# Kernel optimization log

Measured on AMD Instinct MI355X. Metric: run time of the kernel, lower is better.

The kernel has to match this reference:

```python
import jax, jax.numpy as jnp
import numpy as np

B, H, L, D = 2, 16, 1024, 64
LMAX = 2048  # max_sequence_length: patterns built & normalized at LMAX, then sliced to L
PI = float(np.pi)


def _scale_pattern(freq):
    # pattern[h, t, d] = exp(i(t+ph)) + exp(i(2t+ph)) + exp(i(0.5t+ph)), ph = 2*pi*h/H
    # identical across d, so keep [H, L, 1] and broadcast over D
    phase = 2.0 * PI * jnp.arange(H, dtype=jnp.float32) / H          # [H]
    t = jnp.linspace(0.0, 2.0 * PI * freq, LMAX)                     # [LMAX]
    a1 = t[None, :] + phase[:, None]
    a2 = 2.0 * t[None, :] + phase[:, None]
    a3 = 0.5 * t[None, :] + phase[:, None]
    pr = jnp.cos(a1) + jnp.cos(a2) + jnp.cos(a3)                     # [H, LMAX]
    pi_ = jnp.sin(a1) + jnp.sin(a2) + jnp.sin(a3)
    norm = jnp.sqrt(jnp.sum(pr * pr + pi_ * pi_, axis=1, keepdims=True))  # over full LMAX
    pr, pi_ = pr / norm, pi_ / norm
    return pr[:, :L, None], pi_[:, :L, None]                          # [H, L, 1]


def _expert_total_pattern():
    # 8 experts x 3 aspects; pattern[t, d] = exp(i(f*t + 2*pi*d/D)), normalized per
    # column over LMAX (|exp|=1 -> norm sqrt(LMAX)). Elementwise complex multiply is
    # linear, so the expert stage equals x * sum(all patterns)/(sqrt(3)*sqrt(8)).
    freqs = np.array([[0.3 + 0.1 * i, 0.2 + 0.1 * i, 0.1 + 0.1 * i]
                      for i in range(8)], dtype=np.float32).reshape(-1)   # [24]
    t = jnp.linspace(0.0, 2.0 * PI, LMAX)                                 # [LMAX]
    phase_d = 2.0 * PI * jnp.arange(D, dtype=jnp.float32) / D             # [D]
    ang = jnp.asarray(freqs)[:, None, None] * t[None, :, None] + phase_d[None, None, :]  # [24, LMAX, D]
    col_norm = 1.0 / np.sqrt(float(LMAX))
    denom = np.sqrt(3.0) * np.sqrt(8.0)
    pr = jnp.sum(jnp.cos(ang), axis=0) * (col_norm / denom)               # [LMAX, D]
    pi_ = jnp.sum(jnp.sin(ang), axis=0) * (col_norm / denom)
    return pr[:L], pi_[:L]                                                # [L, D]


def _process_scale(Qr, Qi, Kr, Ki, Vr, Vi, pr, pi_):
    # complex elementwise pattern multiply
    Qpr = Qr * pr - Qi * pi_
    Qpi = Qr * pi_ + Qi * pr
    Kpr = Kr * pr - Ki * pi_
    Kpi = Kr * pi_ + Ki * pr
    # complex scores = Qp @ Kp^T (no conjugation, matching the torch code)
    sr = jnp.einsum('bhld,bhmd->bhlm', Qpr, Kpr) - jnp.einsum('bhld,bhmd->bhlm', Qpi, Kpi)
    si = jnp.einsum('bhld,bhmd->bhlm', Qpr, Kpi) + jnp.einsum('bhld,bhmd->bhlm', Qpi, Kpr)
    mag = jnp.sqrt(sr * sr + si * si) / np.sqrt(float(D))
    w = jax.nn.softmax(mag, axis=-1)
    return (jnp.einsum('bhlm,bhmd->bhld', w, Vr),
            jnp.einsum('bhlm,bhmd->bhld', w, Vi))


def reference(Q_real, Q_imag, K_real, K_imag, V_real, V_imag):
    scale_freqs = [1.0, 0.5, 0.25, 0.1]  # char, word, phrase, sentence
    acc_r = jnp.zeros_like(Q_real)
    acc_i = jnp.zeros_like(Q_real)
    for f in scale_freqs:
        pr, pi_ = _scale_pattern(f)
        o_r, o_i = _process_scale(Q_real, Q_imag, K_real, K_imag, V_real, V_imag, pr, pi_)
        acc_r = acc_r + o_r
        acc_i = acc_i + o_i
    inv = 1.0 / np.sqrt(float(len(scale_freqs)))
    acc_r = acc_r * inv
    acc_i = acc_i * inv
    # expert mixing (linear in x -> single fused complex elementwise multiply)
    epr, epi = _expert_total_pattern()  # [L, D], broadcast over B,H
    out_r = acc_r * epr - acc_i * epi
    out_i = acc_r * epi + acc_i * epr
    return jnp.stack([out_r, out_i], axis=0)  # [2, B, H, L, D] (real, imag)


def setup_inputs() -> dict:
    key = jax.random.key(0)
    ks = jax.random.split(key, 6)
    shape = (B, H, L, D)
    names = ['Q_real', 'Q_imag', 'K_real', 'K_imag', 'V_real', 'V_imag']
    return {n: jax.random.normal(k, shape, dtype=jnp.float32) for n, k in zip(names, ks)}
```

## Files before the change

kernel.cpp:

```cpp
#include <hip/hip_runtime.h>
#include <math.h>

typedef short bf16x8 __attribute__((ext_vector_type(8)));
typedef float f32x4 __attribute__((ext_vector_type(4)));

#define BDIM 256
#define ADIM 1024
constexpr int B_ = 2, H_ = 16, L_ = 1024, D_ = 64, LMAX_ = 2048;
constexpr int BH_ = B_ * H_;
constexpr float PI_F = 3.14159265358979323846f;

constexpr int WS_SVP = 0;
constexpr int WS_KBR = 65536;
constexpr int WS_KBI = WS_KBR + 1048576;
constexpr int WS_VTR = WS_KBI + 1048576;
constexpr int WS_VTI = WS_VTR + 1048576;

__device__ __forceinline__ unsigned short f2b(float x) {
    union { float f; unsigned u; } v; v.f = x;
    return (unsigned short)((v.u + 0x8000u) >> 16);
}
__device__ __forceinline__ float b2f(unsigned short x) {
    union { unsigned u; float f; } v; v.u = ((unsigned)x) << 16;
    return v.f;
}
__device__ __forceinline__ unsigned pk2(float a, float b) {
    union { float f; unsigned u; } va, vb; va.f = a; vb.f = b;
    return ((va.u + 0x8000u) >> 16) | ((vb.u + 0x8000u) & 0xFFFF0000u);
}
__device__ __forceinline__ uint4 pack4(const float4& a, const float4& b) {
    return make_uint4(pk2(a.x, a.y), pk2(a.z, a.w), pk2(b.x, b.y), pk2(b.z, b.w));
}
__device__ __forceinline__ unsigned cvtpk(float lo, float hi) {
    unsigned r;
    asm("v_cvt_pk_bf16_f32 %0, %1, %2" : "=v"(r) : "v"(lo), "v"(hi));
    return r;
}
__device__ __forceinline__ float vsqrt(float x) {
    float r;
    asm("v_sqrt_f32 %0, %1" : "=v"(r) : "v"(x));
    return r;
}

#define MFMA(a, b, c) __builtin_amdgcn_mfma_f32_16x16x32_bf16((a), (b), (c), 0, 0, 0)

__device__ __forceinline__ float a_val(int s, int l, float4 invn) {
    const float fr = (s == 0) ? 1.0f : (s == 1) ? 0.5f : (s == 2) ? 0.25f : 0.1f;
    const float iv = (s == 0) ? invn.x : (s == 1) ? invn.y : (s == 2) ? invn.z : invn.w;
    float t = (2.0f * PI_F * fr / (float)(LMAX_ - 1)) * (float)l;
    float m2 = 3.0f + 2.0f * cosf(t) + 2.0f * cosf(0.5f * t) + 2.0f * cosf(1.5f * t);
    return sqrtf(fmaxf(m2, 0.0f)) * iv;
}

__global__ __launch_bounds__(BDIM)
void prep_kernel(const float* __restrict__ Kr, const float* __restrict__ Ki,
                 const float* __restrict__ Vr, const float* __restrict__ Vi,
                 float* __restrict__ ws) {
    const int tid = threadIdx.x;
    const int blk = blockIdx.x;
    unsigned short* KbR = (unsigned short*)(ws + WS_KBR);
    unsigned short* KbI = (unsigned short*)(ws + WS_KBI);
    unsigned short* VtR = (unsigned short*)(ws + WS_VTR);
    unsigned short* VtI = (unsigned short*)(ws + WS_VTI);

    if (blk < 256) {
        const int comp = blk >> 7;
        const float* src = comp ? Ki : Kr;
        unsigned short* dst = comp ? KbI : KbR;
        size_t b0 = (size_t)(blk & 127) * 16384;
#pragma unroll
        for (int i = 0; i < 4; ++i) {
            size_t e = b0 + (size_t)(i * 256 + tid) * 16;
            float4 x0 = *(const float4*)(src + e);
            float4 x1 = *(const float4*)(src + e + 4);
            float4 x2 = *(const float4*)(src + e + 8);
            float4 x3 = *(const float4*)(src + e + 12);
            *(uint4*)(dst + e) = pack4(x0, x1);
            *(uint4*)(dst + e + 8) = pack4(x2, x3);
        }
    } else {
        __shared__ unsigned short sT[64 * 70];
        __shared__ float sRed[4 * 64];
        const int vb = blk - 256;
        const int comp = vb & 1, mt = (vb >> 1) & 15, bh = vb >> 5;
        const int m0 = mt * 64;
        const float* src = (comp ? Vi : Vr) + (size_t)bh * 65536 + (size_t)m0 * 64;
        unsigned short* dstA = (comp ? VtI : VtR) + (size_t)bh * 65536;
#pragma unroll
        for (int i = 0; i < 4; ++i) {
            int e = i * 256 + tid;
            int m = e >> 4, d4 = (e & 15) * 4;
            float4 x = *(const float4*)(src + (size_t)m * 64 + d4);
            *(uint2*)&sT[m * 70 + d4] = make_uint2(pk2(x.x, x.y), pk2(x.z, x.w));
        }
        {
            int d = tid & 63, grp = tid >> 6;
            float s = 0.0f;
#pragma unroll
            for (int k = 0; k < 16; ++k) s += src[(size_t)(grp * 16 + k) * 64 + d];
            sRed[grp * 64 + d] = s;
        }
        __syncthreads();
        {
            int d = tid >> 2, ms = (tid & 3) * 16;
            unsigned short v[16];
#pragma unroll
            for (int k = 0; k < 16; ++k) v[k] = sT[(ms + k) * 70 + d];
            unsigned short* dst = dstA + (size_t)d * 1024 + m0 + ms;
            *(uint4*)dst = make_uint4((unsigned)v[0] | ((unsigned)v[1] << 16),
                                      (unsigned)v[2] | ((unsigned)v[3] << 16),
                                      (unsigned)v[4] | ((unsigned)v[5] << 16),
                                      (unsigned)v[6] | ((unsigned)v[7] << 16));
            *(uint4*)(dst + 8) = make_uint4((unsigned)v[8] | ((unsigned)v[9] << 16),
                                            (unsigned)v[10] | ((unsigned)v[11] << 16),
                                            (unsigned)v[12] | ((unsigned)v[13] << 16),
                                            (unsigned)v[14] | ((unsigned)v[15] << 16));
        }
        if (tid < 64)
            ws[WS_SVP + comp * 32768 + bh * 1024 + tid * 16 + mt] =
                sRed[tid] + sRed[64 + tid] + sRed[128 + tid] + sRed[192 + tid];
    }
}

__device__ __forceinline__ void stage64s(const unsigned short* g0, int stride,
                                         unsigned short* lds, int w, int lane) {
#pragma unroll
    for (int i = 0; i < 2; ++i) {
        int c = w * 2 + i;
        int lrow = c * 8 + (lane >> 3);
        int lg = (lane & 7) ^ (lrow & 7);
        const unsigned short* src = g0 + (size_t)lrow * stride + lg * 8;
        __builtin_amdgcn_global_load_lds(
            (const __attribute__((address_space(1))) void*)src,
            (__attribute__((address_space(3))) void*)(lds + c * 512), 16, 0, 0);
    }
}
__device__ __forceinline__ bf16x8 ldfrag(const unsigned short* b, int row, int g) {
    return *(const bf16x8*)&b[row * 64 + ((g ^ (row & 7)) << 3)];
}

constexpr int OFF_DEN = 0;
constexpr int OFF_K0  = 2048;
constexpr int OFF_K1  = OFF_K0 + 16384;
constexpr int OFF_V0  = OFF_K1 + 16384;
constexpr int OFF_V1  = OFF_V0 + 16384;
constexpr int OFF_E   = OFF_V1 + 16384;
constexpr int OFF_MG  = OFF_E + 16384;
constexpr int OFF_AMB = OFF_MG + 16384;
constexpr int SMEM_BYTES = OFF_AMB + 8256;

__global__ __launch_bounds__(ADIM, 1)
void attn_kernel_w(const float* __restrict__ Qr, const float* __restrict__ Qi,
                   const float* __restrict__ ws, float* __restrict__ out, float4 invn) {
    extern __shared__ char smem[];
    float* sDen = (float*)(smem + OFF_DEN);
    unsigned short* sK0 = (unsigned short*)(smem + OFF_K0);
    unsigned short* sK1 = (unsigned short*)(smem + OFF_K1);
    unsigned short* sV0 = (unsigned short*)(smem + OFF_V0);
    unsigned short* sV1 = (unsigned short*)(smem + OFF_V1);
    unsigned short* sE  = (unsigned short*)(smem + OFF_E);
    unsigned short* sMg = (unsigned short*)(smem + OFF_MG);
    unsigned short* sAmb = (unsigned short*)(smem + OFF_AMB);

    const int tid = threadIdx.x;
    const int lane = tid & 63;
    const int w = tid >> 6;
    const int half = w >> 3;
    const int w8 = w & 7;
    const int lo16 = lane & 15;
    const int quad = lane >> 4;
    const int gh = quad + half * 4;
    const int blk = blockIdx.x;
    const int bh = (blk & 7) * 4 + (blk >> 6);
    const int qt = (blk >> 3) & 7;
    const int l0 = qt * 128;
    const size_t base = (size_t)bh * (L_ * D_);

    const unsigned short* gKr = (const unsigned short*)(ws + WS_KBR) + (size_t)bh * 65536;
    const unsigned short* gKi = (const unsigned short*)(ws + WS_KBI) + (size_t)bh * 65536;
    const unsigned short* gVr = (const unsigned short*)(ws + WS_VTR) + (size_t)bh * 65536;
    const unsigned short* gVi = (const unsigned short*)(ws + WS_VTI) + (size_t)bh * 65536;

    if (w < 4) {
        stage64s(gKr, 64, sK0, w, lane);
        stage64s(gKi, 64, sK1, w, lane);
    } else if (w >= 8 && w < 12) {
        stage64s(gVr, 1024, sV0, w - 8, lane);
        stage64s(gVi, 1024, sV1, w - 8, lane);
    }

    for (int e = tid; e < 4096; e += ADIM) {
        int s = e >> 10, l = e & 1023;
        sAmb[s * 1032 + l] = f2b(a_val(s, l, invn) * 0.125f);
    }

    bf16x8 fQr0, fQr1, fQi0, fQi1, fnQi0, fnQi1;
    {
        const int ql = l0 + w8 * 16 + lo16;
        const float* qr = Qr + base + (size_t)ql * 64;
        const float* qi = Qi + base + (size_t)ql * 64;
        float4 a0 = *(const float4*)(qr + quad * 8);
        float4 a1 = *(const float4*)(qr + quad * 8 + 4);
        float4 b0 = *(const float4*)(qr + 32 + quad * 8);
        float4 b1 = *(const float4*)(qr + 32 + quad * 8 + 4);
        *(uint4*)&fQr0 = pack4(a0, a1);
        *(uint4*)&fQr1 = pack4(b0, b1);
        a0 = *(const float4*)(qi + quad * 8);
        a1 = *(const float4*)(qi + quad * 8 + 4);
        b0 = *(const float4*)(qi + 32 + quad * 8);
        b1 = *(const float4*)(qi + 32 + quad * 8 + 4);
        *(uint4*)&fQi0 = pack4(a0, a1);
        *(uint4*)&fQi1 = pack4(b0, b1);
        uint4 t0 = *(uint4*)&fQi0, t1 = *(uint4*)&fQi1;
        t0.x ^= 0x80008000u; t0.y ^= 0x80008000u; t0.z ^= 0x80008000u; t0.w ^= 0x80008000u;
        t1.x ^= 0x80008000u; t1.y ^= 0x80008000u; t1.z ^= 0x80008000u; t1.w ^= 0x80008000u;
        *(uint4*)&fnQi0 = t0; *(uint4*)&fnQi1 = t1;
    }

    __syncthreads();

    bf16x8 uf1a = (bf16x8){0, 0, 0, 0, 0, 0, 0, 0};
    uf1a[0] = (short)f2b(b2f(sAmb[quad * 1032 + (l0 + w8 * 16 + lo16)]) *
                         (1.0f / 128.0f));

    f32x4 accM1 = (f32x4){0.f, 0.f, 0.f, 0.f};
    f32x4 aOutR[4], aOutI[4];
#pragma unroll
    for (int dt = 0; dt < 4; ++dt) {
        aOutR[dt] = (f32x4){0.f, 0.f, 0.f, 0.f};
        aOutI[dt] = (f32x4){0.f, 0.f, 0.f, 0.f};
    }

    const int lrow_w = w8 * 16 + lo16;

#pragma unroll 1
    for (int mt = 0; mt < 16; ++mt) {
        const int m0 = mt * 64;
        const int cur = mt & 1;
        if (mt < 15) {
            if (w < 4) {
                stage64s(gKr + (size_t)(m0 + 64) * 64, 64, sK0 + (cur ^ 1) * 4096, w, lane);
                stage64s(gKi + (size_t)(m0 + 64) * 64, 64, sK1 + (cur ^ 1) * 4096, w, lane);
            } else if (w >= 8 && w < 12) {
                stage64s(gVr + m0 + 64, 1024, sV0 + (cur ^ 1) * 4096, w - 8, lane);
                stage64s(gVi + m0 + 64, 1024, sV1 + (cur ^ 1) * 4096, w - 8, lane);
            }
        }
        const unsigned short* cK0 = sK0 + cur * 4096;
        const unsigned short* cK1 = sK1 + cur * 4096;
        const unsigned short* cV0 = sV0 + cur * 4096;
        const unsigned short* cV1 = sV1 + cur * 4096;

#pragma unroll
        for (int ct = 0; ct < 2; ++ct) {
            const int ct_eff = half * 2 + ct;
            const int mrow = ct_eff * 16 + lo16;
            bf16x8 kr0 = ldfrag(cK0, mrow, quad), kr1 = ldfrag(cK0, mrow, quad + 4);
            bf16x8 ki0 = ldfrag(cK1, mrow, quad), ki1 = ldfrag(cK1, mrow, quad + 4);
            f32x4 aR = (f32x4){0.f, 0.f, 0.f, 0.f};
            f32x4 aI = (f32x4){0.f, 0.f, 0.f, 0.f};
            __builtin_amdgcn_s_setprio(1);
            aR = MFMA(kr0, fQr0, aR);  aR = MFMA(kr1, fQr1, aR);
            aR = MFMA(ki0, fnQi0, aR); aR = MFMA(ki1, fnQi1, aR);
            aI = MFMA(ki0, fQr0, aI);  aI = MFMA(ki1, fQr1, aI);
            aI = MFMA(kr0, fQi0, aI);  aI = MFMA(kr1, fQi1, aI);
            __builtin_amdgcn_s_setprio(0);
            float mg0 = vsqrt(fmaf(aR[0], aR[0], aI[0] * aI[0]));
            float mg1 = vsqrt(fmaf(aR[1], aR[1], aI[1] * aI[1]));
            float mg2 = vsqrt(fmaf(aR[2], aR[2], aI[2] * aI[2]));
            float mg3 = vsqrt(fmaf(aR[3], aR[3], aI[3] * aI[3]));
            bf16x8 bf1 = (bf16x8){0, 0, 0, 0, 0, 0, 0, 0};
            bf1[0] = (short)sAmb[quad * 1032 + m0 + ct_eff * 16 + lo16];
            f32x4 z = (f32x4){0.f, 0.f, 0.f, 0.f};
            f32x4 a1 = MFMA(bf1, uf1a, z);
            float p0 = mg0 * a1[0], p1 = mg1 * a1[1];
            float p2 = mg2 * a1[2], p3 = mg3 * a1[3];
            int gph = (ct_eff * 2 + (quad >> 1)) ^ (lrow_w & 7);
            *(uint2*)&sE[lrow_w * 64 + gph * 8 + (quad & 1) * 4] =
                make_uint2(cvtpk(p0, p1), cvtpk(p2, p3));
            *(uint2*)&sMg[lrow_w * 64 + gph * 8 + (quad & 1) * 4] =
                make_uint2(cvtpk(mg0, mg1), cvtpk(mg2, mg3));
        }
        {
            bf16x8 mf = ldfrag(sMg, lrow_w, gh);
            bf16x8 b0 = (bf16x8){0, 0, 0, 0, 0, 0, 0, 0};
            if (lo16 < 4)
                b0 = *(const bf16x8*)&sAmb[lo16 * 1032 + m0 + half * 32 + quad * 8];
            accM1 = MFMA(mf, b0, accM1);
        }
        {
            bf16x8 pa = ldfrag(sE, lrow_w, gh);
            __builtin_amdgcn_s_setprio(1);
#pragma unroll
            for (int dt = 0; dt < 4; ++dt) {
                int dr = dt * 16 + lo16;
                bf16x8 vr = ldfrag(cV0, dr, gh);
                bf16x8 vi = ldfrag(cV1, dr, gh);
                aOutR[dt] = MFMA(pa, vr, aOutR[dt]);
                aOutI[dt] = MFMA(pa, vi, aOutI[dt]);
            }
            __builtin_amdgcn_s_setprio(0);
        }
        asm volatile("s_waitcnt vmcnt(0)" ::: "memory");
        __builtin_amdgcn_s_barrier();
    }

    char* scr = smem + OFF_K0;
    if (half == 1) {
#pragma unroll
        for (int dt = 0; dt < 4; ++dt) {
            *(f32x4*)(scr + w8 * 9216 + dt * 1024 + lane * 16) = aOutR[dt];
            *(f32x4*)(scr + w8 * 9216 + 4096 + dt * 1024 + lane * 16) = aOutI[dt];
        }
        *(f32x4*)(scr + w8 * 9216 + 8192 + lane * 16) = accM1;
    }
    __syncthreads();
    if (half == 1) return;

#pragma unroll
    for (int dt = 0; dt < 4; ++dt) {
        aOutR[dt] += *(const f32x4*)(scr + w8 * 9216 + dt * 1024 + lane * 16);
        aOutI[dt] += *(const f32x4*)(scr + w8 * 9216 + 4096 + dt * 1024 + lane * 16);
    }
    accM1 += *(const f32x4*)(scr + w8 * 9216 + 8192 + lane * 16);

    if (lo16 < 4) {
#pragma unroll
        for (int reg = 0; reg < 4; ++reg) {
            int r = w8 * 16 + quad * 4 + reg;
            float alv = b2f(sAmb[lo16 * 1032 + (l0 + r)]) * 8.0f;
            sDen[lo16 * 128 + r] = 1.0f / (1024.0f + alv * accM1[reg]);
        }
    }
    float cden[4];
#pragma unroll
    for (int reg = 0; reg < 4; ++reg) {
        int r = w8 * 16 + quad * 4 + reg;
        cden[reg] = sDen[r] + sDen[128 + r] + sDen[256 + r] + sDen[384 + r];
    }

    const float cE = rsqrtf(2048.0f) * rsqrtf(24.0f);
    float eRr[4], eRi[4];
#pragma unroll
    for (int reg = 0; reg < 4; ++reg) {
        int lrow = l0 + w8 * 16 + quad * 4 + reg;
        float tl = (2.0f * PI_F / (float)(LMAX_ - 1)) * (float)lrow;
        float s1, c1;
        __sincosf(0.1f * tl, &s1, &c1);
        const float W[10] = {1.f, 2.f, 3.f, 3.f, 3.f, 3.f, 3.f, 3.f, 2.f, 1.f};
        float cr = c1, ci = s1;
        float er = W[0] * cr, ei = W[0] * ci;
#pragma unroll
        for (int k = 1; k < 10; ++k) {
            float nr = cr * c1 - ci * s1;
            float ni = cr * s1 + ci * c1;
            cr = nr; ci = ni;
            er = fmaf(W[k], cr, er);
            ei = fmaf(W[k], ci, ei);
        }
        eRr[reg] = er * cE;
        eRi[reg] = ei * cE;
    }

    const size_t ooff = (size_t)BH_ * L_ * D_;
#pragma unroll
    for (int dt = 0; dt < 4; ++dt) {
        int d = dt * 16 + lo16;
        const float* svp = ws + WS_SVP + bh * 1024 + (size_t)d * 16;
        float4 r0 = *(const float4*)(svp);
        float4 r1 = *(const float4*)(svp + 4);
        float4 r2 = *(const float4*)(svp + 8);
        float4 r3 = *(const float4*)(svp + 12);
        float svr = (r0.x + r0.y + r0.z + r0.w) + (r1.x + r1.y + r1.z + r1.w) +
                    (r2.x + r2.y + r2.z + r2.w) + (r3.x + r3.y + r3.z + r3.w);
        const float* svq = svp + 32768;
        r0 = *(const float4*)(svq);
        r1 = *(const float4*)(svq + 4);
        r2 = *(const float4*)(svq + 8);
        r3 = *(const float4*)(svq + 12);
        float svi = (r0.x + r0.y + r0.z + r0.w) + (r1.x + r1.y + r1.z + r1.w) +
                    (r2.x + r2.y + r2.z + r2.w) + (r3.x + r3.y + r3.z + r3.w);
        float sp, cp;
        __sincosf((2.0f * PI_F / 64.0f) * (float)d, &sp, &cp);
#pragma unroll
        for (int reg = 0; reg < 4; ++reg) {
            int lrow = l0 + w8 * 16 + quad * 4 + reg;
            float numR = fmaf(cden[reg], svr, aOutR[dt][reg]) * 0.5f;
            float numI = fmaf(cden[reg], svi, aOutI[dt][reg]) * 0.5f;
            float epr = cp * eRr[reg] - sp * eRi[reg];
            float epi = sp * eRr[reg] + cp * eRi[reg];
            size_t o = base + (size_t)lrow * 64 + d;
            out[o] = numR * epr - numI * epi;
            out[o + ooff] = numR * epi + numI * epr;
        }
    }
}

__global__ __launch_bounds__(BDIM, 2)
void attn_kernel(const float* __restrict__ Qr, const float* __restrict__ Qi,
                 const float* __restrict__ ws, float* __restrict__ out, float4 invn) {
    __shared__ unsigned short sK0[2][4096], sK1[2][4096];
    __shared__ unsigned short sV0[4096], sV1[4096];
    __shared__ unsigned short sE[4096];
    __shared__ unsigned short sMg[4096];
    __shared__ unsigned short sAmb[4 * 1032];
    __shared__ float sDen[4 * 64];

    const int tid = threadIdx.x;
    const int lane = tid & 63;
    const int w = tid >> 6;
    const int lo16 = lane & 15;
    const int quad = lane >> 4;
    const int blk = blockIdx.x;
    const int bh = (blk & 7) * 4 + (blk >> 7);
    const int qt = (blk >> 3) & 15;
    const int l0 = qt * 64;
    const size_t base = (size_t)bh * (L_ * D_);

    const unsigned short* gKr = (const unsigned short*)(ws + WS_KBR) + (size_t)bh * 65536;
    const unsigned short* gKi = (const unsigned short*)(ws + WS_KBI) + (size_t)bh * 65536;
    const unsigned short* gVr = (const unsigned short*)(ws + WS_VTR) + (size_t)bh * 65536;
    const unsigned short* gVi = (const unsigned short*)(ws + WS_VTI) + (size_t)bh * 65536;

    stage64s(gKr, 64, sK0[0], w, lane);
    stage64s(gKi, 64, sK1[0], w, lane);

    for (int e = tid; e < 4096; e += BDIM) {
        int s = e >> 10, l = e & 1023;
        sAmb[s * 1032 + l] = f2b(a_val(s, l, invn) * 0.125f);
    }

    bf16x8 fQr0, fQr1, fQi0, fQi1, fnQi0, fnQi1;
    {
        const int ql = l0 + w * 16 + lo16;
        const float* qr = Qr + base + (size_t)ql * 64;
        const float* qi = Qi + base + (size_t)ql * 64;
        float4 a0 = *(const float4*)(qr + quad * 8);
        float4 a1 = *(const float4*)(qr + quad * 8 + 4);
        float4 b0 = *(const float4*)(qr + 32 + quad * 8);
        float4 b1 = *(const float4*)(qr + 32 + quad * 8 + 4);
        *(uint4*)&fQr0 = pack4(a0, a1);
        *(uint4*)&fQr1 = pack4(b0, b1);
        a0 = *(const float4*)(qi + quad * 8);
        a1 = *(const float4*)(qi + quad * 8 + 4);
        b0 = *(const float4*)(qi + 32 + quad * 8);
        b1 = *(const float4*)(qi + 32 + quad * 8 + 4);
        *(uint4*)&fQi0 = pack4(a0, a1);
        *(uint4*)&fQi1 = pack4(b0, b1);
        uint4 t0 = *(uint4*)&fQi0, t1 = *(uint4*)&fQi1;
        t0.x ^= 0x80008000u; t0.y ^= 0x80008000u; t0.z ^= 0x80008000u; t0.w ^= 0x80008000u;
        t1.x ^= 0x80008000u; t1.y ^= 0x80008000u; t1.z ^= 0x80008000u; t1.w ^= 0x80008000u;
        *(uint4*)&fnQi0 = t0; *(uint4*)&fnQi1 = t1;
    }

    __syncthreads();

    bf16x8 uf1a = (bf16x8){0, 0, 0, 0, 0, 0, 0, 0};
    uf1a[0] = (short)f2b(b2f(sAmb[quad * 1032 + (l0 + w * 16 + lo16)]) *
                         (1.0f / 128.0f));

    f32x4 accM1 = (f32x4){0.f, 0.f, 0.f, 0.f};
    f32x4 aOutR[4], aOutI[4];
#pragma unroll
    for (int dt = 0; dt < 4; ++dt) {
        aOutR[dt] = (f32x4){0.f, 0.f, 0.f, 0.f};
        aOutI[dt] = (f32x4){0.f, 0.f, 0.f, 0.f};
    }

#pragma unroll 1
    for (int mt = 0; mt < 16; ++mt) {
        const int m0 = mt * 64;
        const int cur = mt & 1;
        stage64s(gVr + m0, 1024, sV0, w, lane);
        stage64s(gVi + m0, 1024, sV1, w, lane);
        if (mt < 15) {
            stage64s(gKr + (size_t)(m0 + 64) * 64, 64, sK0[cur ^ 1], w, lane);
            stage64s(gKi + (size_t)(m0 + 64) * 64, 64, sK1[cur ^ 1], w, lane);
        }
        const unsigned short* cK0 = sK0[cur];
        const unsigned short* cK1 = sK1[cur];

#pragma unroll
        for (int ct = 0; ct < 4; ++ct) {
            const int mrow = ct * 16 + lo16;
            bf16x8 kr0 = ldfrag(cK0, mrow, quad), kr1 = ldfrag(cK0, mrow, quad + 4);
            bf16x8 ki0 = ldfrag(cK1, mrow, quad), ki1 = ldfrag(cK1, mrow, quad + 4);
            f32x4 aR = (f32x4){0.f, 0.f, 0.f, 0.f};
            f32x4 aI = (f32x4){0.f, 0.f, 0.f, 0.f};
            __builtin_amdgcn_s_setprio(1);
            aR = MFMA(kr0, fQr0, aR);  aR = MFMA(kr1, fQr1, aR);
            aR = MFMA(ki0, fnQi0, aR); aR = MFMA(ki1, fnQi1, aR);
            aI = MFMA(ki0, fQr0, aI);  aI = MFMA(ki1, fQr1, aI);
            aI = MFMA(kr0, fQi0, aI);  aI = MFMA(kr1, fQi1, aI);
            __builtin_amdgcn_s_setprio(0);
            float mg0 = vsqrt(fmaf(aR[0], aR[0], aI[0] * aI[0]));
            float mg1 = vsqrt(fmaf(aR[1], aR[1], aI[1] * aI[1]));
            float mg2 = vsqrt(fmaf(aR[2], aR[2], aI[2] * aI[2]));
            float mg3 = vsqrt(fmaf(aR[3], aR[3], aI[3] * aI[3]));
            bf16x8 bf1 = (bf16x8){0, 0, 0, 0, 0, 0, 0, 0};
            bf1[0] = (short)sAmb[quad * 1032 + m0 + ct * 16 + lo16];
            f32x4 z = (f32x4){0.f, 0.f, 0.f, 0.f};
            f32x4 a1 = MFMA(bf1, uf1a, z);
            float p0 = mg0 * a1[0], p1 = mg1 * a1[1];
            float p2 = mg2 * a1[2], p3 = mg3 * a1[3];
            int l = w * 16 + lo16;
            int gph = (ct * 2 + (quad >> 1)) ^ (l & 7);
            *(uint2*)&sE[l * 64 + gph * 8 + (quad & 1) * 4] =
                make_uint2(cvtpk(p0, p1), cvtpk(p2, p3));
            *(uint2*)&sMg[l * 64 + gph * 8 + (quad & 1) * 4] =
                make_uint2(cvtpk(mg0, mg1), cvtpk(mg2, mg3));
        }
        {
            bf16x8 mf0 = ldfrag(sMg, w * 16 + lo16, quad);
            bf16x8 mf1 = ldfrag(sMg, w * 16 + lo16, quad + 4);
            bf16x8 b0 = (bf16x8){0, 0, 0, 0, 0, 0, 0, 0};
            bf16x8 b1 = (bf16x8){0, 0, 0, 0, 0, 0, 0, 0};
            if (lo16 < 4) {
                b0 = *(const bf16x8*)&sAmb[lo16 * 1032 + m0 + quad * 8];
                b1 = *(const bf16x8*)&sAmb[lo16 * 1032 + m0 + 32 + quad * 8];
            }
            accM1 = MFMA(mf0, b0, accM1);
            accM1 = MFMA(mf1, b1, accM1);
        }
        if (mt < 15) {
            asm volatile("s_waitcnt vmcnt(4)" ::: "memory");
        } else {
            asm volatile("s_waitcnt vmcnt(0)" ::: "memory");
        }
        __builtin_amdgcn_s_barrier();
        {
            bf16x8 pa0 = ldfrag(sE, w * 16 + lo16, quad);
            bf16x8 pa1 = ldfrag(sE, w * 16 + lo16, quad + 4);
            __builtin_amdgcn_s_setprio(1);
#pragma unroll
            for (int dt = 0; dt < 4; ++dt) {
                int dr = dt * 16 + lo16;
                bf16x8 vr0 = ldfrag(sV0, dr, quad), vr1 = ldfrag(sV0, dr, quad + 4);
                bf16x8 vi0 = ldfrag(sV1, dr, quad), vi1 = ldfrag(sV1, dr, quad + 4);
                aOutR[dt] = MFMA(pa0, vr0, aOutR[dt]);
                aOutR[dt] = MFMA(pa1, vr1, aOutR[dt]);
                aOutI[dt] = MFMA(pa0, vi0, aOutI[dt]);
                aOutI[dt] = MFMA(pa1, vi1, aOutI[dt]);
            }
            __builtin_amdgcn_s_setprio(0);
        }
        asm volatile("s_waitcnt vmcnt(0)" ::: "memory");
        __builtin_amdgcn_s_barrier();
    }

    if (lo16 < 4) {
#pragma unroll
        for (int reg = 0; reg < 4; ++reg) {
            int r = w * 16 + quad * 4 + reg;
            float alv = b2f(sAmb[lo16 * 1032 + (l0 + r)]) * 8.0f;
            sDen[lo16 * 64 + r] = 1.0f / (1024.0f + alv * accM1[reg]);
        }
    }
    float cden[4];
#pragma unroll
    for (int reg = 0; reg < 4; ++reg) {
        int r = w * 16 + quad * 4 + reg;
        cden[reg] = sDen[r] + sDen[64 + r] + sDen[128 + r] + sDen[192 + r];
    }

    const float cE = rsqrtf(2048.0f) * rsqrtf(24.0f);
    float eRr[4], eRi[4];
#pragma unroll
    for (int reg = 0; reg < 4; ++reg) {
        int lrow = l0 + w * 16 + quad * 4 + reg;
        float tl = (2.0f * PI_F / (float)(LMAX_ - 1)) * (float)lrow;
        float s1, c1;
        __sincosf(0.1f * tl, &s1, &c1);
        const float W[10] = {1.f, 2.f, 3.f, 3.f, 3.f, 3.f, 3.f, 3.f, 2.f, 1.f};
        float cr = c1, ci = s1;
        float er = W[0] * cr, ei = W[0] * ci;
#pragma unroll
        for (int k = 1; k < 10; ++k) {
            float nr = cr * c1 - ci * s1;
            float ni = cr * s1 + ci * c1;
            cr = nr; ci = ni;
            er = fmaf(W[k], cr, er);
            ei = fmaf(W[k], ci, ei);
        }
        eRr[reg] = er * cE;
        eRi[reg] = ei * cE;
    }

    const size_t ooff = (size_t)BH_ * L_ * D_;
#pragma unroll
    for (int dt = 0; dt < 4; ++dt) {
        int d = dt * 16 + lo16;
        const float* svp = ws + WS_SVP + bh * 1024 + (size_t)d * 16;
        float4 r0 = *(const float4*)(svp);
        float4 r1 = *(const float4*)(svp + 4);
        float4 r2 = *(const float4*)(svp + 8);
        float4 r3 = *(const float4*)(svp + 12);
        float svr = (r0.x + r0.y + r0.z + r0.w) + (r1.x + r1.y + r1.z + r1.w) +
                    (r2.x + r2.y + r2.z + r2.w) + (r3.x + r3.y + r3.z + r3.w);
        const float* svq = svp + 32768;
        r0 = *(const float4*)(svq);
        r1 = *(const float4*)(svq + 4);
        r2 = *(const float4*)(svq + 8);
        r3 = *(const float4*)(svq + 12);
        float svi = (r0.x + r0.y + r0.z + r0.w) + (r1.x + r1.y + r1.z + r1.w) +
                    (r2.x + r2.y + r2.z + r2.w) + (r3.x + r3.y + r3.z + r3.w);
        float sp, cp;
        __sincosf((2.0f * PI_F / 64.0f) * (float)d, &sp, &cp);
#pragma unroll
        for (int reg = 0; reg < 4; ++reg) {
            int lrow = l0 + w * 16 + quad * 4 + reg;
            float numR = fmaf(cden[reg], svr, aOutR[dt][reg]) * 0.5f;
            float numI = fmaf(cden[reg], svi, aOutI[dt][reg]) * 0.5f;
            float epr = cp * eRr[reg] - sp * eRi[reg];
            float epi = sp * eRr[reg] + cp * eRi[reg];
            size_t o = base + (size_t)lrow * 64 + d;
            out[o] = numR * epr - numI * epi;
            out[o + ooff] = numR * epi + numI * epr;
        }
    }
}

extern "C" void kernel_launch(void* const* d_in, const int* in_sizes, int n_in,
                              void* d_out, int out_size, void* d_ws, size_t ws_size,
                              hipStream_t stream) {
    const float* Qr = (const float*)d_in[0];
    const float* Qi = (const float*)d_in[1];
    const float* Kr = (const float*)d_in[2];
    const float* Ki = (const float*)d_in[3];
    const float* Vr = (const float*)d_in[4];
    const float* Vi = (const float*)d_in[5];
    float* ws = (float*)d_ws;
    float* out = (float*)d_out;

    const double fr[4] = {1.0, 0.5, 0.25, 0.1};
    float inv[4];
    for (int s = 0; s < 4; ++s) {
        double a = 2.0 * 3.14159265358979323846 * fr[s] / (double)(LMAX_ - 1);
        double S = 3.0 * LMAX_;
        const double mul[3] = {1.0, 0.5, 1.5};
        for (int k = 0; k < 3; ++k) {
            double x = a * mul[k];
            S += 2.0 * (cos(x * 1023.5) * sin(x * 1024.0) / sin(x * 0.5));
        }
        inv[s] = (float)(1.0 / sqrt(S));
    }
    float4 invn = make_float4(inv[0], inv[1], inv[2], inv[3]);

    prep_kernel<<<1280, BDIM, 0, stream>>>(Kr, Ki, Vr, Vi, ws);

    static int wideOK = -1;
    if (wideOK < 0) {
        hipError_t e = hipFuncSetAttribute(
            reinterpret_cast<const void*>(attn_kernel_w),
            hipFuncAttributeMaxDynamicSharedMemorySize, SMEM_BYTES);
        wideOK = (e == hipSuccess) ? 1 : 0;
    }
    if (wideOK)
        attn_kernel_w<<<256, ADIM, SMEM_BYTES, stream>>>(Qr, Qi, ws, out, invn);
    else
        attn_kernel<<<512, BDIM, 0, stream>>>(Qr, Qi, ws, out, invn);
}
```

Baseline: 134.6 us.

## Halve workgroup to 8 waves, each wave handling two 16-row query subtiles

The wide attention kernel drops from 16 waves to 8 waves per workgroup, and each wave now processes two 16-row query slices. That lets one loaded K fragment and one loaded V fragment feed twice as many MFMAs. Launch bounds now ask for 2 workgroups per CU, so two blocks may be resident at once. The trade-off is roughly doubled accumulator register pressure per wave (two sets of output and score accumulators), which risks spills or lower effective occupancy.

```diff
diff --git a/kernel.cpp b/kernel.cpp
--- a/kernel.cpp
+++ b/kernel.cpp
@@ -5,7 +5,7 @@
 typedef float f32x4 __attribute__((ext_vector_type(4)));
 
 #define BDIM 256
-#define ADIM 1024
+#define ADIM 512
 constexpr int B_ = 2, H_ = 16, L_ = 1024, D_ = 64, LMAX_ = 2048;
 constexpr int BH_ = B_ * H_;
 constexpr float PI_F = 3.14159265358979323846f;
@@ -149,7 +149,7 @@
 constexpr int OFF_AMB = OFF_MG + 16384;
 constexpr int SMEM_BYTES = OFF_AMB + 8256;
 
-__global__ __launch_bounds__(ADIM, 1)
+__global__ __launch_bounds__(ADIM, 2)
 void attn_kernel_w(const float* __restrict__ Qr, const float* __restrict__ Qi,
                    const float* __restrict__ ws, float* __restrict__ out, float4 invn) {
     extern __shared__ char smem[];
@@ -165,8 +165,8 @@
     const int tid = threadIdx.x;
     const int lane = tid & 63;
     const int w = tid >> 6;
-    const int half = w >> 3;
-    const int w8 = w & 7;
+    const int half = w >> 2;
+    const int w4 = w & 3;
     const int lo16 = lane & 15;
     const int quad = lane >> 4;
     const int gh = quad + half * 4;
@@ -184,9 +184,9 @@
     if (w < 4) {
         stage64s(gKr, 64, sK0, w, lane);
         stage64s(gKi, 64, sK1, w, lane);
-    } else if (w >= 8 && w < 12) {
-        stage64s(gVr, 1024, sV0, w - 8, lane);
-        stage64s(gVi, 1024, sV1, w - 8, lane);
+    } else {
+        stage64s(gVr, 1024, sV0, w - 4, lane);
+        stage64s(gVi, 1024, sV1, w - 4, lane);
     }
 
     for (int e = tid; e < 4096; e += ADIM) {
@@ -194,44 +194,51 @@
         sAmb[s * 1032 + l] = f2b(a_val(s, l, invn) * 0.125f);
     }
 
-    bf16x8 fQr0, fQr1, fQi0, fQi1, fnQi0, fnQi1;
-    {
-        const int ql = l0 + w8 * 16 + lo16;
+    bf16x8 fQr0[2], fQr1[2], fQi0[2], fQi1[2], fnQi0[2], fnQi1[2];
+#pragma unroll
+    for (int qs = 0; qs < 2; ++qs) {
+        const int ql = l0 + w4 * 32 + qs * 16 + lo16;
         const float* qr = Qr + base + (size_t)ql * 64;
         const float* qi = Qi + base + (size_t)ql * 64;
         float4 a0 = *(const float4*)(qr + quad * 8);
         float4 a1 = *(const float4*)(qr + quad * 8 + 4);
         float4 b0 = *(const float4*)(qr + 32 + quad * 8);
         float4 b1 = *(const float4*)(qr + 32 + quad * 8 + 4);
-        *(uint4*)&fQr0 = pack4(a0, a1);
-        *(uint4*)&fQr1 = pack4(b0, b1);
+        *(uint4*)&fQr0[qs] = pack4(a0, a1);
+        *(uint4*)&fQr1[qs] = pack4(b0, b1);
         a0 = *(const float4*)(qi + quad * 8);
         a1 = *(const float4*)(qi + quad * 8 + 4);
         b0 = *(const float4*)(qi + 32 + quad * 8);
         b1 = *(const float4*)(qi + 32 + quad * 8 + 4);
-        *(uint4*)&fQi0 = pack4(a0, a1);
-        *(uint4*)&fQi1 = pack4(b0, b1);
-        uint4 t0 = *(uint4*)&fQi0, t1 = *(uint4*)&fQi1;
+        *(uint4*)&fQi0[qs] = pack4(a0, a1);
+        *(uint4*)&fQi1[qs] = pack4(b0, b1);
+        uint4 t0 = *(uint4*)&fQi0[qs], t1 = *(uint4*)&fQi1[qs];
         t0.x ^= 0x80008000u; t0.y ^= 0x80008000u; t0.z ^= 0x80008000u; t0.w ^= 0x80008000u;
         t1.x ^= 0x80008000u; t1.y ^= 0x80008000u; t1.z ^= 0x80008000u; t1.w ^= 0x80008000u;
-        *(uint4*)&fnQi0 = t0; *(uint4*)&fnQi1 = t1;
+        *(uint4*)&fnQi0[qs] = t0; *(uint4*)&fnQi1[qs] = t1;
     }
 
     __syncthreads();
 
-    bf16x8 uf1a = (bf16x8){0, 0, 0, 0, 0, 0, 0, 0};
-    uf1a[0] = (short)f2b(b2f(sAmb[quad * 1032 + (l0 + w8 * 16 + lo16)]) *
-                         (1.0f / 128.0f));
-
-    f32x4 accM1 = (f32x4){0.f, 0.f, 0.f, 0.f};
-    f32x4 aOutR[4], aOutI[4];
-#pragma unroll
-    for (int dt = 0; dt < 4; ++dt) {
-        aOutR[dt] = (f32x4){0.f, 0.f, 0.f, 0.f};
-        aOutI[dt] = (f32x4){0.f, 0.f, 0.f, 0.f};
-    }
-
-    const int lrow_w = w8 * 16 + lo16;
+    bf16x8 uf1a[2];
+#pragma unroll
+    for (int qs = 0; qs < 2; ++qs) {
+        uf1a[qs] = (bf16x8){0, 0, 0, 0, 0, 0, 0, 0};
+        uf1a[qs][0] = (short)f2b(
+            b2f(sAmb[quad * 1032 + (l0 + w4 * 32 + qs * 16 + lo16)]) * (1.0f / 128.0f));
+    }
+
+    f32x4 accM1[2];
+    f32x4 aOutR[2][4], aOutI[2][4];
+#pragma unroll
+    for (int qs = 0; qs < 2; ++qs) {
+        accM1[qs] = (f32x4){0.f, 0.f, 0.f, 0.f};
+#pragma unroll
+        for (int dt = 0; dt < 4; ++dt) {
+            aOutR[qs][dt] = (f32x4){0.f, 0.f, 0.f, 0.f};
+            aOutI[qs][dt] = (f32x4){0.f, 0.f, 0.f, 0.f};
+        }
+    }
 
 #pragma unroll 1
     for (int mt = 0; mt < 16; ++mt) {
@@ -241,9 +248,9 @@
             if (w < 4) {
                 stage64s(gKr + (size_t)(m0 + 64) * 64, 64, sK0 + (cur ^ 1) * 4096, w, lane);
                 stage64s(gKi + (size_t)(m0 + 64) * 64, 64, sK1 + (cur ^ 1) * 4096, w, lane);
-            } else if (w >= 8 && w < 12) {
-                stage64s(gVr + m0 + 64, 1024, sV0 + (cur ^ 1) * 4096, w - 8, lane);
-                stage64s(gVi + m0 + 64, 1024, sV1 + (cur ^ 1) * 4096, w - 8, lane);
+            } else {
+                stage64s(gVr + m0 + 64, 1024, sV0 + (cur ^ 1) * 4096, w - 4, lane);
+                stage64s(gVi + m0 + 64, 1024, sV1 + (cur ^ 1) * 4096, w - 4, lane);
             }
         }
         const unsigned short* cK0 = sK0 + cur * 4096;
@@ -257,47 +264,57 @@
             const int mrow = ct_eff * 16 + lo16;
             bf16x8 kr0 = ldfrag(cK0, mrow, quad), kr1 = ldfrag(cK0, mrow, quad + 4);
             bf16x8 ki0 = ldfrag(cK1, mrow, quad), ki1 = ldfrag(cK1, mrow, quad + 4);
-            f32x4 aR = (f32x4){0.f, 0.f, 0.f, 0.f};
-            f32x4 aI = (f32x4){0.f, 0.f, 0.f, 0.f};
-            __builtin_amdgcn_s_setprio(1);
-            aR = MFMA(kr0, fQr0, aR);  aR = MFMA(kr1, fQr1, aR);
-            aR = MFMA(ki0, fnQi0, aR); aR = MFMA(ki1, fnQi1, aR);
-            aI = MFMA(ki0, fQr0, aI);  aI = MFMA(ki1, fQr1, aI);
-            aI = MFMA(kr0, fQi0, aI);  aI = MFMA(kr1, fQi1, aI);
-            __builtin_amdgcn_s_setprio(0);
-            float mg0 = vsqrt(fmaf(aR[0], aR[0], aI[0] * aI[0]));
-            float mg1 = vsqrt(fmaf(aR[1], aR[1], aI[1] * aI[1]));
-            float mg2 = vsqrt(fmaf(aR[2], aR[2], aI[2] * aI[2]));
-            float mg3 = vsqrt(fmaf(aR[3], aR[3], aI[3] * aI[3]));
             bf16x8 bf1 = (bf16x8){0, 0, 0, 0, 0, 0, 0, 0};
             bf1[0] = (short)sAmb[quad * 1032 + m0 + ct_eff * 16 + lo16];
-            f32x4 z = (f32x4){0.f, 0.f, 0.f, 0.f};
-            f32x4 a1 = MFMA(bf1, uf1a, z);
-            float p0 = mg0 * a1[0], p1 = mg1 * a1[1];
-            float p2 = mg2 * a1[2], p3 = mg3 * a1[3];
-            int gph = (ct_eff * 2 + (quad >> 1)) ^ (lrow_w & 7);
-            *(uint2*)&sE[lrow_w * 64 + gph * 8 + (quad & 1) * 4] =
-                make_uint2(cvtpk(p0, p1), cvtpk(p2, p3));
-            *(uint2*)&sMg[lrow_w * 64 + gph * 8 + (quad & 1) * 4] =
-                make_uint2(cvtpk(mg0, mg1), cvtpk(mg2, mg3));
+#pragma unroll
+            for (int qs = 0; qs < 2; ++qs) {
+                f32x4 aR = (f32x4){0.f, 0.f, 0.f, 0.f};
+                f32x4 aI = (f32x4){0.f, 0.f, 0.f, 0.f};
+                __builtin_amdgcn_s_setprio(1);
+                aR = MFMA(kr0, fQr0[qs], aR);  aR = MFMA(kr1, fQr1[qs], aR);
+                aR = MFMA(ki0, fnQi0[qs], aR); aR = MFMA(ki1, fnQi1[qs], aR);
+                aI = MFMA(ki0, fQr0[qs], aI);  aI = MFMA(ki1, fQr1[qs], aI);
+                aI = MFMA(kr0, fQi0[qs], aI);  aI = MFMA(kr1, fQi1[qs], aI);
+                __builtin_amdgcn_s_setprio(0);
+                float mg0 = vsqrt(fmaf(aR[0], aR[0], aI[0] * aI[0]));
+                float mg1 = vsqrt(fmaf(aR[1], aR[1], aI[1] * aI[1]));
+                float mg2 = vsqrt(fmaf(aR[2], aR[2], aI[2] * aI[2]));
+                float mg3 = vsqrt(fmaf(aR[3], aR[3], aI[3] * aI[3]));
+                f32x4 z = (f32x4){0.f, 0.f, 0.f, 0.f};
+                f32x4 a1 = MFMA(bf1, uf1a[qs], z);
+                float p0 = mg0 * a1[0], p1 = mg1 * a1[1];
+                float p2 = mg2 * a1[2], p3 = mg3 * a1[3];
+                const int lrow = w4 * 32 + qs * 16 + lo16;
+                int gph = (ct_eff * 2 + (quad >> 1)) ^ (lrow & 7);
+                *(uint2*)&sE[lrow * 64 + gph * 8 + (quad & 1) * 4] =
+                    make_uint2(cvtpk(p0, p1), cvtpk(p2, p3));
+                *(uint2*)&sMg[lrow * 64 + gph * 8 + (quad & 1) * 4] =
+                    make_uint2(cvtpk(mg0, mg1), cvtpk(mg2, mg3));
+            }
         }
         {
-            bf16x8 mf = ldfrag(sMg, lrow_w, gh);
             bf16x8 b0 = (bf16x8){0, 0, 0, 0, 0, 0, 0, 0};
             if (lo16 < 4)
                 b0 = *(const bf16x8*)&sAmb[lo16 * 1032 + m0 + half * 32 + quad * 8];
-            accM1 = MFMA(mf, b0, accM1);
+#pragma unroll
+            for (int qs = 0; qs < 2; ++qs) {
+                bf16x8 mf = ldfrag(sMg, w4 * 32 + qs * 16 + lo16, gh);
+                accM1[qs] = MFMA(mf, b0, accM1[qs]);
+            }
         }
         {
-            bf16x8 pa = ldfrag(sE, lrow_w, gh);
+            bf16x8 pa0 = ldfrag(sE, w4 * 32 + lo16, gh);
+            bf16x8 pa1 = ldfrag(sE, w4 * 32 + 16 + lo16, gh);
             __builtin_amdgcn_s_setprio(1);
 #pragma unroll
             for (int dt = 0; dt < 4; ++dt) {
                 int dr = dt * 16 + lo16;
                 bf16x8 vr = ldfrag(cV0, dr, gh);
                 bf16x8 vi = ldfrag(cV1, dr, gh);
-                aOutR[dt] = MFMA(pa, vr, aOutR[dt]);
-                aOutI[dt] = MFMA(pa, vi, aOutI[dt]);
+                aOutR[0][dt] = MFMA(pa0, vr, aOutR[0][dt]);
+                aOutI[0][dt] = MFMA(pa0, vi, aOutI[0][dt]);
+                aOutR[1][dt] = MFMA(pa1, vr, aOutR[1][dt]);
+                aOutI[1][dt] = MFMA(pa1, vi, aOutI[1][dt]);
             }
             __builtin_amdgcn_s_setprio(0);
         }
@@ -308,59 +325,74 @@
     char* scr = smem + OFF_K0;
     if (half == 1) {
 #pragma unroll
-        for (int dt = 0; dt < 4; ++dt) {
-            *(f32x4*)(scr + w8 * 9216 + dt * 1024 + lane * 16) = aOutR[dt];
-            *(f32x4*)(scr + w8 * 9216 + 4096 + dt * 1024 + lane * 16) = aOutI[dt];
-        }
-        *(f32x4*)(scr + w8 * 9216 + 8192 + lane * 16) = accM1;
+        for (int qs = 0; qs < 2; ++qs) {
+            char* s0 = scr + (w4 * 2 + qs) * 9216;
+#pragma unroll
+            for (int dt = 0; dt < 4; ++dt) {
+                *(f32x4*)(s0 + dt * 1024 + lane * 16) = aOutR[qs][dt];
+                *(f32x4*)(s0 + 4096 + dt * 1024 + lane * 16) = aOutI[qs][dt];
+            }
+            *(f32x4*)(s0 + 8192 + lane * 16) = accM1[qs];
+        }
     }
     __syncthreads();
     if (half == 1) return;
 
 #pragma unroll
-    for (int dt = 0; dt < 4; ++dt) {
-        aOutR[dt] += *(const f32x4*)(scr + w8 * 9216 + dt * 1024 + lane * 16);
-        aOutI[dt] += *(const f32x4*)(scr + w8 * 9216 + 4096 + dt * 1024 + lane * 16);
-    }
-    accM1 += *(const f32x4*)(scr + w8 * 9216 + 8192 + lane * 16);
-
-    if (lo16 < 4) {
+    for (int qs = 0; qs < 2; ++qs) {
+        char* s0 = scr + (w4 * 2 + qs) * 9216;
+#pragma unroll
+        for (int dt = 0; dt < 4; ++dt) {
+            aOutR[qs][dt] += *(const f32x4*)(s0 + dt * 1024 + lane * 16);
+            aOutI[qs][dt] += *(const f32x4*)(s0 + 4096 + dt * 1024 + lane * 16);
+        }
+        accM1[qs] += *(const f32x4*)(s0 + 8192 + lane * 16);
+    }
+
+#pragma unroll
+    for (int qs = 0; qs < 2; ++qs) {
+        if (lo16 < 4) {
+#pragma unroll
+            for (int reg = 0; reg < 4; ++reg) {
+                int r = w4 * 32 + qs * 16 + quad * 4 + reg;
+                float alv = b2f(sAmb[lo16 * 1032 + (l0 + r)]) * 8.0f;
+                sDen[lo16 * 128 + r] = 1.0f / (1024.0f + alv * accM1[qs][reg]);
+            }
+        }
+    }
+    float cden[2][4];
+#pragma unroll
+    for (int qs = 0; qs < 2; ++qs)
 #pragma unroll
         for (int reg = 0; reg < 4; ++reg) {
-            int r = w8 * 16 + quad * 4 + reg;
-            float alv = b2f(sAmb[lo16 * 1032 + (l0 + r)]) * 8.0f;
-            sDen[lo16 * 128 + r] = 1.0f / (1024.0f + alv * accM1[reg]);
-        }
-    }
-    float cden[4];
-#pragma unroll
-    for (int reg = 0; reg < 4; ++reg) {
-        int r = w8 * 16 + quad * 4 + reg;
-        cden[reg] = sDen[r] + sDen[128 + r] + sDen[256 + r] + sDen[384 + r];
-    }
+            int r = w4 * 32 + qs * 16 + quad * 4 + reg;
+            cden[qs][reg] = sDen[r] + sDen[128 + r] + sDen[256 + r] + sDen[384 + r];
+        }
 
     const float cE = rsqrtf(2048.0f) * rsqrtf(24.0f);
-    float eRr[4], eRi[4];
-#pragma unroll
-    for (int reg = 0; reg < 4; ++reg) {
-        int lrow = l0 + w8 * 16 + quad * 4 + reg;
-        float tl = (2.0f * PI_F / (float)(LMAX_ - 1)) * (float)lrow;
-        float s1, c1;
-        __sincosf(0.1f * tl, &s1, &c1);
-        const float W[10] = {1.f, 2.f, 3.f, 3.f, 3.f, 3.f, 3.f, 3.f, 2.f, 1.f};
-        float cr = c1, ci = s1;
-        float er = W[0] * cr, ei = W[0] * ci;
-#pragma unroll
-        for (int k = 1; k < 10; ++k) {
-            float nr = cr * c1 - ci * s1;
-            float ni = cr * s1 + ci * c1;
-            cr = nr; ci = ni;
-            er = fmaf(W[k], cr, er);
-            ei = fmaf(W[k], ci, ei);
-        }
-        eRr[reg] = er * cE;
-        eRi[reg] = ei * cE;
-    }
+    float eRr[2][4], eRi[2][4];
+#pragma unroll
+    for (int qs = 0; qs < 2; ++qs)
+#pragma unroll
+        for (int reg = 0; reg < 4; ++reg) {
+            int lrow = l0 + w4 * 32 + qs * 16 + quad * 4 + reg;
+            float tl = (2.0f * PI_F / (float)(LMAX_ - 1)) * (float)lrow;
+            float s1, c1;
+            __sincosf(0.1f * tl, &s1, &c1);
+            const float W[10] = {1.f, 2.f, 3.f, 3.f, 3.f, 3.f, 3.f, 3.f, 2.f, 1.f};
+            float cr = c1, ci = s1;
+            float er = W[0] * cr, ei = W[0] * ci;
+#pragma unroll
+            for (int k = 1; k < 10; ++k) {
+                float nr = cr * c1 - ci * s1;
+                float ni = cr * s1 + ci * c1;
+                cr = nr; ci = ni;
+                er = fmaf(W[k], cr, er);
+                ei = fmaf(W[k], ci, ei);
+            }
+            eRr[qs][reg] = er * cE;
+            eRi[qs][reg] = ei * cE;
+        }
 
     const size_t ooff = (size_t)BH_ * L_ * D_;
 #pragma unroll
@@ -383,16 +415,18 @@
         float sp, cp;
         __sincosf((2.0f * PI_F / 64.0f) * (float)d, &sp, &cp);
 #pragma unroll
-        for (int reg = 0; reg < 4; ++reg) {
-            int lrow = l0 + w8 * 16 + quad * 4 + reg;
-            float numR = fmaf(cden[reg], svr, aOutR[dt][reg]) * 0.5f;
-            float numI = fmaf(cden[reg], svi, aOutI[dt][reg]) * 0.5f;
-            float epr = cp * eRr[reg] - sp * eRi[reg];
-            float epi = sp * eRr[reg] + cp * eRi[reg];
-            size_t o = base + (size_t)lrow * 64 + d;
-            out[o] = numR * epr - numI * epi;
-            out[o + ooff] = numR * epi + numI * epr;
-        }
+        for (int qs = 0; qs < 2; ++qs)
+#pragma unroll
+            for (int reg = 0; reg < 4; ++reg) {
+                int lrow = l0 + w4 * 32 + qs * 16 + quad * 4 + reg;
+                float numR = fmaf(cden[qs][reg], svr, aOutR[qs][dt][reg]) * 0.5f;
+                float numI = fmaf(cden[qs][reg], svi, aOutI[qs][dt][reg]) * 0.5f;
+                float epr = cp * eRr[qs][reg] - sp * eRi[qs][reg];
+                float epi = sp * eRr[qs][reg] + cp * eRi[qs][reg];
+                size_t o = base + (size_t)lrow * 64 + d;
+                out[o] = numR * epr - numI * epi;
+                out[o + ooff] = numR * epi + numI * epr;
+            }
     }
 }
 
```

New measurement: 136.0 us. No clear change (+1.1%).
